# Optimization experiments

Hardware: AMD Instinct MI355X
Metric: run time of the kernel (lower is better)

## Reference

```python
import jax, jax.numpy as jnp
import numpy as np

WINDOW = 512
STEP = 256
N_FREQ = 256
EPS = 1e-8


def setup_inputs() -> dict:
    key = jax.random.key(0)
    k1, k2, k3 = jax.random.split(key, 3)
    audio = jax.random.normal(k1, (512, 32768), dtype=jnp.float32)
    basis_real = jax.random.normal(k2, (N_FREQ, WINDOW), dtype=jnp.float32)
    basis_imag = jax.random.normal(k3, (N_FREQ, WINDOW), dtype=jnp.float32)
    return {"audio": audio, "basis_real": basis_real, "basis_imag": basis_imag}


def reference(audio, basis_real, basis_imag):
    # --- framing (windowed_audio): strided unfold -> [B, n_frames, WINDOW] ---
    n_samples = audio.shape[-1]
    n_frames = (n_samples - WINDOW) // STEP + 1  # 127 for 32768 samples
    idx = jnp.arange(n_frames)[:, None] * STEP + jnp.arange(WINDOW)[None, :]
    windowed = audio[:, idx]  # [B, F, W]

    # --- per-frame L2 normalization ---
    norms = jnp.linalg.norm(windowed, axis=-1, keepdims=True)  # [B, F, 1]
    wn = windowed / (norms + EPS)

    # --- basis normalization by complex L2 norm over window dim ---
    bnorm = jnp.sqrt(jnp.sum(basis_real * basis_real + basis_imag * basis_imag,
                             axis=-1, keepdims=True))  # [K, 1]
    br = basis_real / (bnorm + EPS)
    bi = basis_imag / (bnorm + EPS)

    # --- projection: windowed @ basis.T, real and imag parts ---
    real = jnp.einsum('bfw,kw->bfk', wn, br)  # [B, F, K]
    imag = jnp.einsum('bfw,kw->bfk', wn, bi)  # [B, F, K]
    return norms, real, imag
```

## Files before the change

### kernel.cpp

```cpp
#include <hip/hip_runtime.h>

#define WINDOW   512
#define STEPSZ   256
#define NFRAMES  127
#define NSAMP    32768
#define NBATCH   512
#define NFREQ    256
#define BM       64
#define SAMP_TILE 16640
#define NPS      65

typedef __attribute__((ext_vector_type(8))) short short8;
typedef __attribute__((ext_vector_type(4))) float f32x4;
typedef __attribute__((ext_vector_type(4))) float f4;

#define SWZ(byt) ((byt) ^ ((((byt) >> 9) & 7) << 6))

static __device__ __forceinline__ short f2bf(float x) {
    union { float f; unsigned u; } v; v.f = x;
    unsigned r = (v.u + 0x7fffu + ((v.u >> 16) & 1u)) >> 16;
    return (short)r;
}

__global__ __launch_bounds__(256) void prep_kernel(const float* __restrict__ br,
                                                   const float* __restrict__ bi,
                                                   short* __restrict__ Bf) {
    const int lane = threadIdx.x & 63;
    const int wid  = threadIdx.x >> 6;
    const int k    = blockIdx.x * 4 + wid;
    const float* pr = br + (size_t)k * WINDOW + lane * 8;
    const float* pi = bi + (size_t)k * WINDOW + lane * 8;
    f4 r0 = *(const f4*)pr;
    f4 r1 = *(const f4*)(pr + 4);
    f4 i0 = *(const f4*)pi;
    f4 i1 = *(const f4*)(pi + 4);
    float ss = 0.f;
#pragma unroll
    for (int j = 0; j < 4; ++j)
        ss += r0[j]*r0[j] + r1[j]*r1[j] + i0[j]*i0[j] + i1[j]*i1[j];
#pragma unroll
    for (int d = 1; d < 64; d <<= 1) ss += __shfl_xor(ss, d, 64);
    const float inv = 1.0f / (sqrtf(ss) + 1e-8f);
    short8 hr, hi;
#pragma unroll
    for (int j = 0; j < 4; ++j) {
        hr[j]     = f2bf(r0[j] * inv);
        hr[j + 4] = f2bf(r1[j] * inv);
        hi[j]     = f2bf(i0[j] * inv);
        hi[j + 4] = f2bf(i1[j] * inv);
    }
    const int kk = lane >> 2, kgrp = lane & 3;
    const int rl  = k & 15;
    const int ntR = k >> 4;
    const int ntI = 16 + (k >> 4);
    *(short8*)(Bf + ((size_t)(ntR * 16 + kk) * 64 + kgrp * 16 + rl) * 8) = hr;
    *(short8*)(Bf + ((size_t)(ntI * 16 + kk) * 64 + kgrp * 16 + rl) * 8) = hi;
}

__global__ __launch_bounds__(1024, 4) void mel_kernel(const float* __restrict__ audio,
                                                      const short* __restrict__ Bf,
                                                      float* __restrict__ out) {
    __shared__ short smp[SAMP_TILE];
    __shared__ float ps[NPS];
    __shared__ float invn[BM];

    const int tid  = threadIdx.x;
    const int lane = tid & 63;
    const int wid  = tid >> 6;

    const int b   = blockIdx.x >> 1;
    const int mt0 = blockIdx.x & 1;
    const int f0  = mt0 * BM;

    float* out_norms = out;
    float* out_real  = out + 65024;
    float* out_imag  = out + 65024 + 16646144;

    const float* abase = audio + (size_t)b * NSAMP + f0 * STEPSZ;
    const int smax = NSAMP - f0 * STEPSZ - 8;

    const int rlane = lane & 15;
    const int kgrp  = lane >> 4;
    const int ntg0  = wid * 2;
    const short* bp0 = Bf + ((size_t)(ntg0 + 0) * 16 * 64 + lane) * 8;
    const short* bp1 = Bf + ((size_t)(ntg0 + 1) * 16 * 64 + lane) * 8;

    short8 bb[3][2];
#pragma unroll
    for (int d = 0; d < 3; ++d) {
        bb[d][0] = *(const short8*)(bp0 + (size_t)d * 512);
        bb[d][1] = *(const short8*)(bp1 + (size_t)d * 512);
    }

#pragma unroll
    for (int it = 0; it < 3; ++it) {
        const int sl = it * 8192 + tid * 8;
        float ss = 0.f;
        if (sl < SAMP_TILE) {
            const int slc = sl < smax ? sl : smax;
            f4 v0 = *(const f4*)(abase + slc);
            f4 v1 = *(const f4*)(abase + slc + 4);
            short8 h;
#pragma unroll
            for (int q = 0; q < 4; ++q) {
                ss += v0[q]*v0[q] + v1[q]*v1[q];
                h[q]     = f2bf(v0[q]);
                h[q + 4] = f2bf(v1[q]);
            }
            const int byt = sl * 2;
            *(short8*)((char*)smp + SWZ(byt)) = h;
        }
        ss += __shfl_xor(ss, 1, 64);
        ss += __shfl_xor(ss, 2, 64);
        ss += __shfl_xor(ss, 4, 64);
        ss += __shfl_xor(ss, 8, 64);
        ss += __shfl_xor(ss, 16, 64);
        const int chunk = (it * 8192 + tid * 8) >> 8;
        if ((tid & 31) == 0 && chunk < NPS) ps[chunk] = ss;
    }
    __syncthreads();

    if (tid < BM) {
        const float nrm = sqrtf(ps[tid] + ps[tid + 1]);
        const int fr = f0 + tid;
        if (fr < NFRAMES) out_norms[b * NFRAMES + fr] = nrm;
        invn[tid] = 1.0f / (nrm + 1e-8f);
    }

    const int rb = rlane * 512 + kgrp * 16;
    const int X0 = (rlane & 7) << 6;
    const int X1 = ((rlane + 1) & 7) << 6;
    const char* sb = (const char*)smp;

    f32x4 acc[4][2];
#pragma unroll
    for (int mt = 0; mt < 4; ++mt) { acc[mt][0] = (f32x4)0.f; acc[mt][1] = (f32x4)0.f; }

#pragma unroll
    for (int kk = 0; kk < 16; ++kk) {
        const int X  = (kk < 8) ? X0 : X1;
        const int kb = kk * 64;
        short8 a0 = *(const short8*)(sb + ((rb + 0 * 8192 + kb) ^ X));
        short8 a1 = *(const short8*)(sb + ((rb + 1 * 8192 + kb) ^ X));
        short8 a2 = *(const short8*)(sb + ((rb + 2 * 8192 + kb) ^ X));
        short8 a3 = *(const short8*)(sb + ((rb + 3 * 8192 + kb) ^ X));
        const int cur = kk % 3;
        short8 cb0 = bb[cur][0];
        short8 cb1 = bb[cur][1];
        if (kk < 13) {
            bb[cur][0] = *(const short8*)(bp0 + (size_t)(kk + 3) * 512);
            bb[cur][1] = *(const short8*)(bp1 + (size_t)(kk + 3) * 512);
        }
        acc[0][0] = __builtin_amdgcn_mfma_f32_16x16x32_bf16(a0, cb0, acc[0][0], 0, 0, 0);
        acc[1][0] = __builtin_amdgcn_mfma_f32_16x16x32_bf16(a1, cb0, acc[1][0], 0, 0, 0);
        acc[2][0] = __builtin_amdgcn_mfma_f32_16x16x32_bf16(a2, cb0, acc[2][0], 0, 0, 0);
        acc[3][0] = __builtin_amdgcn_mfma_f32_16x16x32_bf16(a3, cb0, acc[3][0], 0, 0, 0);
        acc[0][1] = __builtin_amdgcn_mfma_f32_16x16x32_bf16(a0, cb1, acc[0][1], 0, 0, 0);
        acc[1][1] = __builtin_amdgcn_mfma_f32_16x16x32_bf16(a1, cb1, acc[1][1], 0, 0, 0);
        acc[2][1] = __builtin_amdgcn_mfma_f32_16x16x32_bf16(a2, cb1, acc[2][1], 0, 0, 0);
        acc[3][1] = __builtin_amdgcn_mfma_f32_16x16x32_bf16(a3, cb1, acc[3][1], 0, 0, 0);
    }
    __syncthreads();

#pragma unroll
    for (int mt = 0; mt < 4; ++mt) {
        const int rbase = mt * 16 + kgrp * 4;
#pragma unroll
        for (int nt = 0; nt < 2; ++nt) {
            const int n = (ntg0 + nt) * 16 + rlane;
            float* dst = (n < NFREQ) ? out_real : out_imag;
            const int kcol = n & (NFREQ - 1);
#pragma unroll
            for (int j = 0; j < 4; ++j) {
                const int r  = rbase + j;
                const int fr = f0 + r;
                if (fr < NFRAMES)
                    dst[((size_t)b * NFRAMES + fr) * NFREQ + kcol] = acc[mt][nt][j] * invn[r];
            }
        }
    }
}

extern "C" void kernel_launch(void* const* d_in, const int* in_sizes, int n_in,
                              void* d_out, int out_size, void* d_ws, size_t ws_size,
                              hipStream_t stream) {
    const float* audio = (const float*)d_in[0];
    const float* br    = (const float*)d_in[1];
    const float* bi    = (const float*)d_in[2];
    float* out = (float*)d_out;
    short* Bf  = (short*)d_ws;

    prep_kernel<<<64, 256, 0, stream>>>(br, bi, Bf);
    mel_kernel<<<NBATCH * 2, 1024, 0, stream>>>(audio, Bf, out);
}
```

Measured before the change: 66.92 us.

## Halve block to 512 threads with 4 N-tiles per wave and new LDS swizzle

Each wave now computes a 64x64 output tile (4 N-tiles) instead of 64x32, so the block shrinks to 512 threads and each A fragment read from LDS feeds twice as many MFMAs. Basis fragments use double buffering (even/odd registers) instead of a three-deep ring, and the LDS XOR swizzle moves from 64-byte to 16-byte granularity. The aim is less LDS traffic per MFMA and fewer bank conflicts, at the cost of more accumulator registers and fewer waves to hide load latency.

```diff
diff --git a/kernel.cpp b/kernel.cpp
--- a/kernel.cpp
+++ b/kernel.cpp
@@ -14,7 +14,7 @@
 typedef __attribute__((ext_vector_type(4))) float f32x4;
 typedef __attribute__((ext_vector_type(4))) float f4;
 
-#define SWZ(byt) ((byt) ^ ((((byt) >> 9) & 7) << 6))
+#define SWZ(byt) ((byt) ^ ((((byt) >> 9) & 7) << 4))
 
 static __device__ __forceinline__ short f2bf(float x) {
     union { float f; unsigned u; } v; v.f = x;
@@ -57,9 +57,27 @@
     *(short8*)(Bf + ((size_t)(ntI * 16 + kk) * 64 + kgrp * 16 + rl) * 8) = hi;
 }
 
-__global__ __launch_bounds__(1024, 4) void mel_kernel(const float* __restrict__ audio,
-                                                      const short* __restrict__ Bf,
-                                                      float* __restrict__ out) {
+#define MFMA16(AB)                                                                  \
+    acc[0][0] = __builtin_amdgcn_mfma_f32_16x16x32_bf16(a0, AB##0, acc[0][0], 0, 0, 0); \
+    acc[1][0] = __builtin_amdgcn_mfma_f32_16x16x32_bf16(a1, AB##0, acc[1][0], 0, 0, 0); \
+    acc[2][0] = __builtin_amdgcn_mfma_f32_16x16x32_bf16(a2, AB##0, acc[2][0], 0, 0, 0); \
+    acc[3][0] = __builtin_amdgcn_mfma_f32_16x16x32_bf16(a3, AB##0, acc[3][0], 0, 0, 0); \
+    acc[0][1] = __builtin_amdgcn_mfma_f32_16x16x32_bf16(a0, AB##1, acc[0][1], 0, 0, 0); \
+    acc[1][1] = __builtin_amdgcn_mfma_f32_16x16x32_bf16(a1, AB##1, acc[1][1], 0, 0, 0); \
+    acc[2][1] = __builtin_amdgcn_mfma_f32_16x16x32_bf16(a2, AB##1, acc[2][1], 0, 0, 0); \
+    acc[3][1] = __builtin_amdgcn_mfma_f32_16x16x32_bf16(a3, AB##1, acc[3][1], 0, 0, 0); \
+    acc[0][2] = __builtin_amdgcn_mfma_f32_16x16x32_bf16(a0, AB##2, acc[0][2], 0, 0, 0); \
+    acc[1][2] = __builtin_amdgcn_mfma_f32_16x16x32_bf16(a1, AB##2, acc[1][2], 0, 0, 0); \
+    acc[2][2] = __builtin_amdgcn_mfma_f32_16x16x32_bf16(a2, AB##2, acc[2][2], 0, 0, 0); \
+    acc[3][2] = __builtin_amdgcn_mfma_f32_16x16x32_bf16(a3, AB##2, acc[3][2], 0, 0, 0); \
+    acc[0][3] = __builtin_amdgcn_mfma_f32_16x16x32_bf16(a0, AB##3, acc[0][3], 0, 0, 0); \
+    acc[1][3] = __builtin_amdgcn_mfma_f32_16x16x32_bf16(a1, AB##3, acc[1][3], 0, 0, 0); \
+    acc[2][3] = __builtin_amdgcn_mfma_f32_16x16x32_bf16(a2, AB##3, acc[2][3], 0, 0, 0); \
+    acc[3][3] = __builtin_amdgcn_mfma_f32_16x16x32_bf16(a3, AB##3, acc[3][3], 0, 0, 0);
+
+__global__ __launch_bounds__(512, 4) void mel_kernel(const float* __restrict__ audio,
+                                                     const short* __restrict__ Bf,
+                                                     float* __restrict__ out) {
     __shared__ short smp[SAMP_TILE];
     __shared__ float ps[NPS];
     __shared__ float invn[BM];
@@ -69,8 +87,8 @@
     const int wid  = tid >> 6;
 
     const int b   = blockIdx.x >> 1;
-    const int mt0 = blockIdx.x & 1;
-    const int f0  = mt0 * BM;
+    const int mh  = blockIdx.x & 1;
+    const int f0  = mh * BM;
 
     float* out_norms = out;
     float* out_real  = out + 65024;
@@ -81,20 +99,21 @@
 
     const int rlane = lane & 15;
     const int kgrp  = lane >> 4;
-    const int ntg0  = wid * 2;
+    const int ntg0  = wid * 4;
+
     const short* bp0 = Bf + ((size_t)(ntg0 + 0) * 16 * 64 + lane) * 8;
     const short* bp1 = Bf + ((size_t)(ntg0 + 1) * 16 * 64 + lane) * 8;
-
-    short8 bb[3][2];
-#pragma unroll
-    for (int d = 0; d < 3; ++d) {
-        bb[d][0] = *(const short8*)(bp0 + (size_t)d * 512);
-        bb[d][1] = *(const short8*)(bp1 + (size_t)d * 512);
-    }
-
-#pragma unroll
-    for (int it = 0; it < 3; ++it) {
-        const int sl = it * 8192 + tid * 8;
+    const short* bp2 = Bf + ((size_t)(ntg0 + 2) * 16 * 64 + lane) * 8;
+    const short* bp3 = Bf + ((size_t)(ntg0 + 3) * 16 * 64 + lane) * 8;
+
+    short8 e0 = *(const short8*)bp0, e1 = *(const short8*)bp1,
+           e2 = *(const short8*)bp2, e3 = *(const short8*)bp3;
+    short8 o0 = *(const short8*)(bp0 + 512), o1 = *(const short8*)(bp1 + 512),
+           o2 = *(const short8*)(bp2 + 512), o3 = *(const short8*)(bp3 + 512);
+
+#pragma unroll
+    for (int it = 0; it < 5; ++it) {
+        const int sl = it * 4096 + tid * 8;
         float ss = 0.f;
         if (sl < SAMP_TILE) {
             const int slc = sl < smax ? sl : smax;
@@ -115,7 +134,7 @@
         ss += __shfl_xor(ss, 4, 64);
         ss += __shfl_xor(ss, 8, 64);
         ss += __shfl_xor(ss, 16, 64);
-        const int chunk = (it * 8192 + tid * 8) >> 8;
+        const int chunk = (it * 4096 + tid * 8) >> 8;
         if ((tid & 31) == 0 && chunk < NPS) ps[chunk] = ss;
     }
     __syncthreads();
@@ -128,13 +147,15 @@
     }
 
     const int rb = rlane * 512 + kgrp * 16;
-    const int X0 = (rlane & 7) << 6;
-    const int X1 = ((rlane + 1) & 7) << 6;
+    const int X0 = (rlane & 7) << 4;
+    const int X1 = ((rlane + 1) & 7) << 4;
     const char* sb = (const char*)smp;
 
-    f32x4 acc[4][2];
-#pragma unroll
-    for (int mt = 0; mt < 4; ++mt) { acc[mt][0] = (f32x4)0.f; acc[mt][1] = (f32x4)0.f; }
+    f32x4 acc[4][4];
+#pragma unroll
+    for (int mt = 0; mt < 4; ++mt)
+#pragma unroll
+        for (int nt = 0; nt < 4; ++nt) acc[mt][nt] = (f32x4)0.f;
 
 #pragma unroll
     for (int kk = 0; kk < 16; ++kk) {
@@ -144,21 +165,23 @@
         short8 a1 = *(const short8*)(sb + ((rb + 1 * 8192 + kb) ^ X));
         short8 a2 = *(const short8*)(sb + ((rb + 2 * 8192 + kb) ^ X));
         short8 a3 = *(const short8*)(sb + ((rb + 3 * 8192 + kb) ^ X));
-        const int cur = kk % 3;
-        short8 cb0 = bb[cur][0];
-        short8 cb1 = bb[cur][1];
-        if (kk < 13) {
-            bb[cur][0] = *(const short8*)(bp0 + (size_t)(kk + 3) * 512);
-            bb[cur][1] = *(const short8*)(bp1 + (size_t)(kk + 3) * 512);
+        if ((kk & 1) == 0) {
+            MFMA16(e)
+            if (kk < 14) {
+                e0 = *(const short8*)(bp0 + (size_t)(kk + 2) * 512);
+                e1 = *(const short8*)(bp1 + (size_t)(kk + 2) * 512);
+                e2 = *(const short8*)(bp2 + (size_t)(kk + 2) * 512);
+                e3 = *(const short8*)(bp3 + (size_t)(kk + 2) * 512);
+            }
+        } else {
+            MFMA16(o)
+            if (kk < 14) {
+                o0 = *(const short8*)(bp0 + (size_t)(kk + 2) * 512);
+                o1 = *(const short8*)(bp1 + (size_t)(kk + 2) * 512);
+                o2 = *(const short8*)(bp2 + (size_t)(kk + 2) * 512);
+                o3 = *(const short8*)(bp3 + (size_t)(kk + 2) * 512);
+            }
         }
-        acc[0][0] = __builtin_amdgcn_mfma_f32_16x16x32_bf16(a0, cb0, acc[0][0], 0, 0, 0);
-        acc[1][0] = __builtin_amdgcn_mfma_f32_16x16x32_bf16(a1, cb0, acc[1][0], 0, 0, 0);
-        acc[2][0] = __builtin_amdgcn_mfma_f32_16x16x32_bf16(a2, cb0, acc[2][0], 0, 0, 0);
-        acc[3][0] = __builtin_amdgcn_mfma_f32_16x16x32_bf16(a3, cb0, acc[3][0], 0, 0, 0);
-        acc[0][1] = __builtin_amdgcn_mfma_f32_16x16x32_bf16(a0, cb1, acc[0][1], 0, 0, 0);
-        acc[1][1] = __builtin_amdgcn_mfma_f32_16x16x32_bf16(a1, cb1, acc[1][1], 0, 0, 0);
-        acc[2][1] = __builtin_amdgcn_mfma_f32_16x16x32_bf16(a2, cb1, acc[2][1], 0, 0, 0);
-        acc[3][1] = __builtin_amdgcn_mfma_f32_16x16x32_bf16(a3, cb1, acc[3][1], 0, 0, 0);
     }
     __syncthreads();
 
@@ -166,7 +189,7 @@
     for (int mt = 0; mt < 4; ++mt) {
         const int rbase = mt * 16 + kgrp * 4;
 #pragma unroll
-        for (int nt = 0; nt < 2; ++nt) {
+        for (int nt = 0; nt < 4; ++nt) {
             const int n = (ntg0 + nt) * 16 + rlane;
             float* dst = (n < NFREQ) ? out_real : out_imag;
             const int kcol = n & (NFREQ - 1);
@@ -191,5 +214,5 @@
     short* Bf  = (short*)d_ws;
 
     prep_kernel<<<64, 256, 0, stream>>>(br, bi, Bf);
-    mel_kernel<<<NBATCH * 2, 1024, 0, stream>>>(audio, Bf, out);
-}
+    mel_kernel<<<NBATCH * 2, 512, 0, stream>>>(audio, Bf, out);
+}
```

Result: slower. 109.7 us (+64.0%).
